# Optimization experiments

Measured on AMD Instinct MI355X. Metric: run time of the kernel, lower is better.

The kernel has to match this reference:

```python
import jax, jax.numpy as jnp
import numpy as np


def setup_inputs() -> dict:
    key = jax.random.key(0)
    ks = jax.random.split(key, 5)
    B, Cin, Cout, H, W, L, K = 16, 512, 512, 64, 64, 512, 3
    return {
        "content": jax.random.normal(ks[0], (B, Cin, H, W), jnp.float32),
        "latent": jax.random.normal(ks[1], (B, L), jnp.float32),
        "noise": jax.random.normal(ks[2], (B, 1, H, W), jnp.float32),
        "affine_w": jax.random.normal(ks[3], (Cin, L), jnp.float32),
        "affine_b": jnp.ones((Cin,), jnp.float32),  # ConvLayer fills affine bias with 1
        "conv_w": jax.random.normal(ks[4], (Cout, Cin, K, K), jnp.float32),
        "bias": jnp.zeros((1, Cout, 1, 1), jnp.float32),
        "noise_weight": jnp.asarray(0.1, jnp.float32),  # nonzero so noise path is exercised
    }


def reference(content, latent, noise, affine_w, affine_b, conv_w, bias, noise_weight):
    L = affine_w.shape[1]
    # affine (LinearLayer, lrelu=False): weight scaled by sqrt(1/inChannels), lrMultiplier=1
    style = latent @ (affine_w * np.sqrt(1.0 / L)).T + affine_b  # [B, Cin]
    # modulate: per-sample weights [B, Cout, Cin, k, k]
    w = conv_w[None] * style[:, None, :, None, None]
    # demodulate
    norm = jax.lax.rsqrt(jnp.sum(jnp.square(w), axis=(2, 3, 4), keepdims=True) + 1e-8)
    w = w * norm
    pad = conv_w.shape[-1] // 2
    # groups=batch trick == per-sample conv; vmap over batch
    def conv1(x, wk):  # x: [Cin,H,W], wk: [Cout,Cin,k,k]
        return jax.lax.conv_general_dilated(x[None], wk, (1, 1), [(pad, pad), (pad, pad)])[0]
    out = jax.vmap(conv1)(content, w)  # [B, Cout, H, W]
    out = out + noise_weight * noise
    out = jax.nn.leaky_relu(out + bias, negative_slope=0.2) * np.sqrt(2.0)
    return out
```

## Files before the change

### kernel.cpp

```cpp
#include <hip/hip_runtime.h>
#include <hip/hip_bf16.h>


typedef float f32x4 __attribute__((ext_vector_type(4)));
typedef float f32x16 __attribute__((ext_vector_type(16)));
typedef short bf16x8 __attribute__((ext_vector_type(8)));
typedef int i32x4 __attribute__((ext_vector_type(4)));

#define BB 16
#define CIN 512
#define COUT 512
#define HH 64
#define WW 64
#define LL 512

#define X3ROWB 2176
#define X3C16B (66 * X3ROWB)
#define X3BB (32 * X3C16B)
#define XS3_SZ (16 * X3BB)

#define WT3_STEPB 147456
#define WT3_SZ (32 * WT3_STEPB)

#define XS3_OFF 0
#define WT3_OFF XS3_SZ
#define STYLE_OFF (WT3_OFF + WT3_SZ)
#define STYLE_SZ (BB * CIN * 4)
#define WSQ_OFF (STYLE_OFF + STYLE_SZ)
#define WSQ_SZ (COUT * CIN * 4)
#define DEM_OFF (WSQ_OFF + WSQ_SZ)
#define DEM_SZ (BB * COUT * 4)
#define WS_NEEDED (DEM_OFF + DEM_SZ)

#define XSTEPB 22528
#define WSTEPB 18432

__device__ __forceinline__ void gld_lds16(const void* g, void* l) {
  __builtin_amdgcn_global_load_lds(
      (const __attribute__((address_space(1))) unsigned int*)g,
      (__attribute__((address_space(3))) unsigned int*)l, 16, 0, 0);
}

__global__ void style_kernel(const float* __restrict__ latent,
                             const float* __restrict__ affine_w,
                             const float* __restrict__ affine_b,
                             float* __restrict__ style) {
  const int idx = blockIdx.x * 256 + threadIdx.x;
  const int b = idx >> 9, ci = idx & 511;
  const float* lp = latent + b * LL;
  const float* wp = affine_w + ci * LL;
  float acc = 0.f;
  for (int l = 0; l < LL; ++l) acc += lp[l] * wp[l];
  style[idx] = acc * 0.044194173824159216f + affine_b[ci];
}

__global__ void wprep_kernel(const float* __restrict__ conv_w,
                             float* __restrict__ wsq,
                             __hip_bfloat16* __restrict__ wt3) {
  const int idx = blockIdx.x * 256 + threadIdx.x;
  const int co = idx >> 9, ci = idx & 511;
  const float* wp = conv_w + idx * 9;
  const int cib = ci >> 4, h = (ci >> 3) & 1, ci8 = ci & 7;
  __hip_bfloat16* base = wt3 + (size_t)cib * 73728 + h * 4096 + co * 8 + ci8;
  float ss = 0.f;
#pragma unroll
  for (int t = 0; t < 9; ++t) {
    float v = wp[t];
    ss += v * v;
    base[t * 8192] = __float2bfloat16(v);
  }
  wsq[idx] = ss;
}

__global__ void dem_kernel(const float* __restrict__ wsq,
                           const float* __restrict__ style,
                           float* __restrict__ dem) {
  const int idx = blockIdx.x * 256 + threadIdx.x;
  const int b = idx >> 9, co = idx & 511;
  const float* sp = style + b * CIN;
  const float* wp = wsq + co * CIN;
  float acc = 0.f;
  for (int ci = 0; ci < CIN; ++ci) {
    float s = sp[ci];
    acc += wp[ci] * s * s;
  }
  dem[idx] = 1.0f / sqrtf(acc + 1e-8f);
}

__global__ void xsprep_kernel(const float* __restrict__ content,
                              const float* __restrict__ style,
                              char* __restrict__ xs3) {
  __shared__ float tile[64][65];
  const int b = blockIdx.x >> 6;
  const int y = blockIdx.x & 63;
  const int tid = threadIdx.x;
  char* bbase = xs3 + (size_t)b * X3BB;

  {
    const int c16 = tid >> 3, rest = tid & 7;
    const int h = rest >> 2, pp = rest & 3;
    const int px = (pp == 0) ? 0 : 64 + pp;
    *(i32x4*)(bbase + (size_t)c16 * X3C16B + (y + 1) * X3ROWB + h * 1088 +
              px * 16) = (i32x4){0, 0, 0, 0};
  }
  if (y == 0 || y == 63) {
    const int rowidx = (y == 0) ? 0 : 65;
#pragma unroll
    for (int k = 0; k < 17; ++k) {
      const int u = tid + k * 256;
      if (u < 4352) {
        const int c16 = u / 136, w = u - c16 * 136;
        *(i32x4*)(bbase + (size_t)c16 * X3C16B + rowidx * X3ROWB + w * 16) =
            (i32x4){0, 0, 0, 0};
      }
    }
  }

  for (int cb = 0; cb < 8; ++cb) {
    const int ci0 = cb * 64;
    __syncthreads();
    {
      const int x = tid & 63;
      const int c0 = tid >> 6;
#pragma unroll
      for (int p = 0; p < 16; ++p) {
        const int ci = p * 4 + c0;
        tile[ci][x] = content[((b * CIN + ci0 + ci) * HH + y) * WW + x];
      }
    }
    __syncthreads();
    {
      const int x = tid & 63;
      const int o4 = tid >> 6;
#pragma unroll
      for (int oo = 0; oo < 2; ++oo) {
        const int oct = o4 * 2 + oo;
        const int c16 = cb * 4 + (oct >> 1);
        const int h = oct & 1;
        bf16x8 v;
#pragma unroll
        for (int j = 0; j < 8; ++j) {
          const float st = style[b * CIN + ci0 + oct * 8 + j];
          v[j] = __bfloat16_as_short(
              __float2bfloat16(tile[oct * 8 + j][x] * st));
        }
        *(bf16x8*)(bbase + (size_t)c16 * X3C16B + (y + 1) * X3ROWB + h * 1088 +
                   (x + 1) * 16) = v;
      }
    }
  }
}

__global__ __launch_bounds__(256, 2) void conv_kernel(
    const char* __restrict__ xs3,
    const char* __restrict__ wt3,
    const float* __restrict__ dem,
    const float* __restrict__ noise,
    const float* __restrict__ biasp,
    const float* __restrict__ nwp,
    float* __restrict__ out) {
  __shared__ __attribute__((aligned(16))) char xlds[2][XSTEPB];
  __shared__ __attribute__((aligned(16))) char wlds[2][WSTEPB];

  const int tid = threadIdx.x;
  const int lane = tid & 63;
  const int wv = tid >> 6;
  const int l31 = lane & 31;
  const int hsel = lane >> 5;

  const int d = blockIdx.x;
  const int L = (d & 7) * 128 + (d >> 3);
  const int cot = L & 7;
  const int yo = (L >> 3) & 7;
  const int b = L >> 6;
  const int co0 = cot << 6;
  const int y0 = yo << 3;

  const char* xsrc[6];
#pragma unroll
  for (int k = 0; k < 6; ++k) {
    const int c = wv + 4 * k;
    if (c < 22) {
      const int beta = c * 1024 + lane * 16;
      const int row = beta / X3ROWB;
      const int within = beta - row * X3ROWB;
      xsrc[k] = xs3 + (size_t)(b * 32) * X3C16B +
                (size_t)(y0 + row) * X3ROWB + within;
    } else {
      xsrc[k] = xs3;
    }
  }
  const char* wsrc[5];
#pragma unroll
  for (int k = 0; k < 5; ++k) {
    const int c = wv + 4 * k;
    if (c < 18) {
      const int tap = c >> 1, h = c & 1;
      wsrc[k] = wt3 + tap * 16384 + h * 8192 + (co0 + lane) * 16;
    } else {
      wsrc[k] = wt3;
    }
  }

  const int abase0 = hsel * 1024 + l31 * 16;
  const int bbase0 = hsel * 1088 + l31 * 16;
  const int xwrow = 2 * wv * X3ROWB;

  f32x16 acc[2][2][2];
#pragma unroll
  for (int mf = 0; mf < 2; ++mf)
#pragma unroll
    for (int r = 0; r < 2; ++r)
#pragma unroll
      for (int q = 0; q < 2; ++q)
#pragma unroll
        for (int e = 0; e < 16; ++e) acc[mf][r][q][e] = 0.f;

#define STG_X(K)                                                        \
  if ((K) < 5 || wv < 2)                                                \
    gld_lds16(xsrc[K] + xadv, xd + (wv + 4 * (K)) * 1024);
#define STG_W(K)                                                        \
  if ((K) < 4 || wv < 2)                                                \
    gld_lds16(wsrc[K] + wadv, wd + (wv + 4 * (K)) * 1024);

  {
    char* xd = xlds[0];
    char* wd = wlds[0];
    const size_t xadv = 0, wadv = 0;
    STG_X(0) STG_X(1) STG_X(2) STG_X(3) STG_X(4) STG_X(5)
    STG_W(0) STG_W(1) STG_W(2) STG_W(3) STG_W(4)
  }
  asm volatile("s_waitcnt vmcnt(0)" ::: "memory");
  __builtin_amdgcn_s_barrier();

#define PHASE(DX, STGPART, TAIL)                                          \
  {                                                                       \
    bf16x8 aP[3][2], bP[4][2];                                            \
    _Pragma("unroll") for (int dy = 0; dy < 3; ++dy)                      \
        _Pragma("unroll") for (int mf = 0; mf < 2; ++mf)                  \
            aP[dy][mf] = *(const bf16x8*)(wb + (dy * 3 + (DX)) * 2048 +   \
                                          abase0 + mf * 512);             \
    _Pragma("unroll") for (int ir = 0; ir < 4; ++ir)                      \
        _Pragma("unroll") for (int q = 0; q < 2; ++q)                     \
            bP[ir][q] = *(const bf16x8*)(xb + xwrow + ir * X3ROWB +       \
                                         bbase0 + (q * 32 + (DX)) * 16);  \
    if (t < 31) { STGPART }                                               \
    __builtin_amdgcn_s_barrier();                                         \
    asm volatile("s_waitcnt lgkmcnt(0)" ::: "memory");                    \
    __builtin_amdgcn_sched_barrier(0);                                    \
    __builtin_amdgcn_s_setprio(1);                                        \
    _Pragma("unroll") for (int ir = 0; ir < 4; ++ir)                      \
        _Pragma("unroll") for (int dy = 0; dy < 3; ++dy) {                \
      const int rr = ir - dy;                                             \
      if (rr == 0 || rr == 1) {                                           \
        _Pragma("unroll") for (int q = 0; q < 2; ++q)                     \
            _Pragma("unroll") for (int mf = 0; mf < 2; ++mf)              \
                acc[mf][rr][q] = __builtin_amdgcn_mfma_f32_32x32x16_bf16( \
                    aP[dy][mf], bP[ir][q], acc[mf][rr][q], 0, 0, 0);      \
      }                                                                   \
    }                                                                     \
    __builtin_amdgcn_s_setprio(0);                                        \
    TAIL;                                                                 \
    __builtin_amdgcn_s_barrier();                                         \
  }

  for (int t = 0; t < 32; ++t) {
    const int bi = t & 1;
    const char* xb = xlds[bi];
    const char* wb = wlds[bi];
    char* xd = xlds[bi ^ 1];
    char* wd = wlds[bi ^ 1];
    const size_t xadv = (size_t)(t + 1) * X3C16B;
    const size_t wadv = (size_t)(t + 1) * WT3_STEPB;

    PHASE(0, STG_X(0) STG_X(1) STG_W(0) STG_W(1), )
    PHASE(1, STG_X(2) STG_X(3) STG_W(2) STG_W(3), )
    PHASE(2, STG_X(4) STG_X(5) STG_W(4),
          asm volatile("s_waitcnt vmcnt(0)" ::: "memory"))
  }
#undef PHASE
#undef STG_X
#undef STG_W

  const float nwv = nwp[0];
  float nz[2][2];
#pragma unroll
  for (int r = 0; r < 2; ++r) {
    const int y = y0 + 2 * wv + r;
#pragma unroll
    for (int q = 0; q < 2; ++q)
      nz[r][q] = nwv * noise[(b << 12) + (y << 6) + q * 32 + l31];
  }
#pragma unroll
  for (int mf = 0; mf < 2; ++mf)
#pragma unroll
    for (int reg = 0; reg < 16; ++reg) {
      const int coo = (reg & 3) + 8 * (reg >> 2) + 4 * hsel;
      const int co = co0 + mf * 32 + coo;
      const float dv = dem[(b << 9) + co];
      const float bv = biasp[co];
#pragma unroll
      for (int r = 0; r < 2; ++r) {
        const int y = y0 + 2 * wv + r;
#pragma unroll
        for (int q = 0; q < 2; ++q) {
          float v = acc[mf][r][q][reg] * dv + nz[r][q] + bv;
          v = (v > 0.f ? v : 0.2f * v) * 1.41421356237309515f;
          out[(((size_t)(b << 9) + co) << 12) + (y << 6) + q * 32 + l31] = v;
        }
      }
    }
}

extern "C" void kernel_launch(void* const* d_in, const int* in_sizes, int n_in,
                              void* d_out, int out_size, void* d_ws, size_t ws_size,
                              hipStream_t stream) {
  const float* content  = (const float*)d_in[0];
  const float* latent   = (const float*)d_in[1];
  const float* noise    = (const float*)d_in[2];
  const float* affine_w = (const float*)d_in[3];
  const float* affine_b = (const float*)d_in[4];
  const float* conv_w   = (const float*)d_in[5];
  const float* bias     = (const float*)d_in[6];
  const float* nw       = (const float*)d_in[7];
  float* out = (float*)d_out;
  char* ws = (char*)d_ws;

  if (ws_size < (size_t)WS_NEEDED) return;

  char* xs3 = ws + XS3_OFF;
  __hip_bfloat16* wt3 = (__hip_bfloat16*)(ws + WT3_OFF);
  float* style = (float*)(ws + STYLE_OFF);
  float* wsq   = (float*)(ws + WSQ_OFF);
  float* dem   = (float*)(ws + DEM_OFF);

  style_kernel<<<dim3(32), dim3(256), 0, stream>>>(latent, affine_w, affine_b, style);
  wprep_kernel<<<dim3(1024), dim3(256), 0, stream>>>(conv_w, wsq, wt3);
  dem_kernel<<<dim3(32), dim3(256), 0, stream>>>(wsq, style, dem);
  xsprep_kernel<<<dim3(1024), dim3(256), 0, stream>>>(content, style, xs3);
  conv_kernel<<<dim3(1024), dim3(256), 0, stream>>>(
      xs3, (const char*)(ws + WT3_OFF), dem, noise, bias, nw, out);
}
```

Before: 316.6 us.

## Software-pipeline LDS fragment reads with register double buffering in conv loop

Restructures the main conv loop so LDS fragment reads for the next dx phase are issued into a second register set while MFMAs consume the current one. Partial lgkmcnt waits replace full drains. All global-to-LDS staging for a step is issued in one batch, and a barrier is dropped per phase. Launch bounds go from two blocks per CU to one, giving the compiler room for the extra fragment registers at the risk of lower occupancy and less latency hiding across blocks.

```diff
diff --git a/kernel.cpp b/kernel.cpp
--- a/kernel.cpp
+++ b/kernel.cpp
@@ -151,7 +151,7 @@
   }
 }
 
-__global__ __launch_bounds__(256, 2) void conv_kernel(
+__global__ __launch_bounds__(256, 1) void conv_kernel(
     const char* __restrict__ xs3,
     const char* __restrict__ wt3,
     const float* __restrict__ dem,
@@ -206,6 +206,11 @@
   const int bbase0 = hsel * 1088 + l31 * 16;
   const int xwrow = 2 * wv * X3ROWB;
 
+  const char* xb0 = xlds[0];
+  const char* wb0 = wlds[0];
+  const char* xb1 = xlds[1];
+  const char* wb1 = wlds[1];
+
   f32x16 acc[2][2][2];
 #pragma unroll
   for (int mf = 0; mf < 2; ++mf)
@@ -216,71 +221,113 @@
 #pragma unroll
         for (int e = 0; e < 16; ++e) acc[mf][r][q][e] = 0.f;
 
-#define STG_X(K)                                                        \
-  if ((K) < 5 || wv < 2)                                                \
-    gld_lds16(xsrc[K] + xadv, xd + (wv + 4 * (K)) * 1024);
-#define STG_W(K)                                                        \
-  if ((K) < 4 || wv < 2)                                                \
-    gld_lds16(wsrc[K] + wadv, wd + (wv + 4 * (K)) * 1024);
+#define STG_ALL                                                     \
+  {                                                                 \
+    _Pragma("unroll") for (int k = 0; k < 6; ++k) {                 \
+      const int c = wv + 4 * k;                                     \
+      if (c < 22) gld_lds16(xsrc[k] + xadv, xd + c * 1024);         \
+    }                                                               \
+    _Pragma("unroll") for (int k = 0; k < 5; ++k) {                 \
+      const int c = wv + 4 * k;                                     \
+      if (c < 18) gld_lds16(wsrc[k] + wadv, wd + c * 1024);         \
+    }                                                               \
+  }
+
+#define RDCL(AA, BB, XB, WB, DX)                                          \
+  {                                                                       \
+    _Pragma("unroll") for (int dy = 0; dy < 3; ++dy)                      \
+        _Pragma("unroll") for (int mf = 0; mf < 2; ++mf)                  \
+            AA[dy][mf] = *(const bf16x8*)((WB) + (dy * 3 + (DX)) * 2048 + \
+                                          abase0 + mf * 512);             \
+    _Pragma("unroll") for (int ir = 0; ir < 4; ++ir)                      \
+        _Pragma("unroll") for (int q = 0; q < 2; ++q)                     \
+            BB[ir][q] = *(const bf16x8*)((XB) + xwrow + ir * X3ROWB +     \
+                                         bbase0 + (q * 32 + (DX)) * 16);  \
+  }                                                                       \
+  __builtin_amdgcn_sched_barrier(0);
+
+#define MMCL(AA, BB)                                                      \
+  _Pragma("unroll") for (int ir = 0; ir < 4; ++ir)                        \
+      _Pragma("unroll") for (int dy = 0; dy < 3; ++dy) {                  \
+    const int rr = ir - dy;                                               \
+    if (rr == 0 || rr == 1) {                                             \
+      _Pragma("unroll") for (int q = 0; q < 2; ++q)                       \
+          _Pragma("unroll") for (int mf = 0; mf < 2; ++mf)                \
+              acc[mf][rr][q] = __builtin_amdgcn_mfma_f32_32x32x16_bf16(   \
+                  AA[dy][mf], BB[ir][q], acc[mf][rr][q], 0, 0, 0);        \
+    }                                                                     \
+  }
+
+#define W14                                                   \
+  asm volatile("s_waitcnt lgkmcnt(14)" ::: "memory");         \
+  __builtin_amdgcn_sched_barrier(0);
+#define WL0                                                   \
+  asm volatile("s_waitcnt lgkmcnt(0)" ::: "memory");          \
+  __builtin_amdgcn_sched_barrier(0);
+#define WV0 asm volatile("s_waitcnt vmcnt(0)" ::: "memory");
+#define BAR __builtin_amdgcn_s_barrier();
 
   {
     char* xd = xlds[0];
     char* wd = wlds[0];
     const size_t xadv = 0, wadv = 0;
-    STG_X(0) STG_X(1) STG_X(2) STG_X(3) STG_X(4) STG_X(5)
-    STG_W(0) STG_W(1) STG_W(2) STG_W(3) STG_W(4)
-  }
-  asm volatile("s_waitcnt vmcnt(0)" ::: "memory");
-  __builtin_amdgcn_s_barrier();
-
-#define PHASE(DX, STGPART, TAIL)                                          \
-  {                                                                       \
-    bf16x8 aP[3][2], bP[4][2];                                            \
-    _Pragma("unroll") for (int dy = 0; dy < 3; ++dy)                      \
-        _Pragma("unroll") for (int mf = 0; mf < 2; ++mf)                  \
-            aP[dy][mf] = *(const bf16x8*)(wb + (dy * 3 + (DX)) * 2048 +   \
-                                          abase0 + mf * 512);             \
-    _Pragma("unroll") for (int ir = 0; ir < 4; ++ir)                      \
-        _Pragma("unroll") for (int q = 0; q < 2; ++q)                     \
-            bP[ir][q] = *(const bf16x8*)(xb + xwrow + ir * X3ROWB +       \
-                                         bbase0 + (q * 32 + (DX)) * 16);  \
-    if (t < 31) { STGPART }                                               \
-    __builtin_amdgcn_s_barrier();                                         \
-    asm volatile("s_waitcnt lgkmcnt(0)" ::: "memory");                    \
-    __builtin_amdgcn_sched_barrier(0);                                    \
-    __builtin_amdgcn_s_setprio(1);                                        \
-    _Pragma("unroll") for (int ir = 0; ir < 4; ++ir)                      \
-        _Pragma("unroll") for (int dy = 0; dy < 3; ++dy) {                \
-      const int rr = ir - dy;                                             \
-      if (rr == 0 || rr == 1) {                                           \
-        _Pragma("unroll") for (int q = 0; q < 2; ++q)                     \
-            _Pragma("unroll") for (int mf = 0; mf < 2; ++mf)              \
-                acc[mf][rr][q] = __builtin_amdgcn_mfma_f32_32x32x16_bf16( \
-                    aP[dy][mf], bP[ir][q], acc[mf][rr][q], 0, 0, 0);      \
-      }                                                                   \
-    }                                                                     \
-    __builtin_amdgcn_s_setprio(0);                                        \
-    TAIL;                                                                 \
-    __builtin_amdgcn_s_barrier();                                         \
-  }
-
-  for (int t = 0; t < 32; ++t) {
-    const int bi = t & 1;
-    const char* xb = xlds[bi];
-    const char* wb = wlds[bi];
-    char* xd = xlds[bi ^ 1];
-    char* wd = wlds[bi ^ 1];
-    const size_t xadv = (size_t)(t + 1) * X3C16B;
-    const size_t wadv = (size_t)(t + 1) * WT3_STEPB;
-
-    PHASE(0, STG_X(0) STG_X(1) STG_W(0) STG_W(1), )
-    PHASE(1, STG_X(2) STG_X(3) STG_W(2) STG_W(3), )
-    PHASE(2, STG_X(4) STG_X(5) STG_W(4),
-          asm volatile("s_waitcnt vmcnt(0)" ::: "memory"))
-  }
-#undef PHASE
-#undef STG_X
-#undef STG_W
+    STG_ALL
+  }
+  WV0;
+  BAR;
+
+  bf16x8 a0[3][2], b0[4][2], a1[3][2], b1[4][2];
+  RDCL(a0, b0, xb0, wb0, 0)
+
+  for (int t = 0; t < 32; t += 2) {
+    RDCL(a1, b1, xb0, wb0, 1)
+    {
+      char* xd = xlds[1];
+      char* wd = wlds[1];
+      const size_t xadv = (size_t)(t + 1) * X3C16B;
+      const size_t wadv = (size_t)(t + 1) * WT3_STEPB;
+      STG_ALL
+    }
+    __builtin_amdgcn_sched_barrier(0);
+    W14 MMCL(a0, b0)
+    RDCL(a0, b0, xb0, wb0, 2)
+    W14 MMCL(a1, b1)
+    WV0;
+    BAR;
+    RDCL(a1, b1, xb1, wb1, 0)
+    W14 MMCL(a0, b0)
+    BAR;
+
+    RDCL(a0, b0, xb1, wb1, 1)
+    if (t < 30) {
+      char* xd = xlds[0];
+      char* wd = wlds[0];
+      const size_t xadv = (size_t)(t + 2) * X3C16B;
+      const size_t wadv = (size_t)(t + 2) * WT3_STEPB;
+      STG_ALL
+    }
+    __builtin_amdgcn_sched_barrier(0);
+    W14 MMCL(a1, b1)
+    RDCL(a1, b1, xb1, wb1, 2)
+    W14 MMCL(a0, b0)
+    WV0;
+    BAR;
+    if (t < 30) {
+      RDCL(a0, b0, xb0, wb0, 0)
+      W14
+    } else {
+      WL0
+    }
+    MMCL(a1, b1)
+    BAR;
+  }
+#undef STG_ALL
+#undef RDCL
+#undef MMCL
+#undef W14
+#undef WL0
+#undef WV0
+#undef BAR
 
   const float nwv = nwp[0];
   float nz[2][2];
```

Measured after the change: 327.7 us. 3.5% more time.

## Double conv block rows to 16 with 512 threads and rewrite xsprep without LDS

Applied to the files above, without the earlier changes.

The conv kernel now uses 512-thread blocks (8 waves) that each cover 16 output rows instead of 8, halving the grid. Each block stages 39 input-row chunks plus the weights, so the weight tile is shared across twice as many rows and the 2-row halo is amortised. All staging for the next step is issued in the first phase, not spread over three. The xsprep kernel drops its shared-memory transpose and reads content with strided loads directly. The cost is larger LDS per block, fewer blocks in flight, and uncoalesced-pattern changes in xsprep.

```diff
diff --git a/kernel.cpp b/kernel.cpp
--- a/kernel.cpp
+++ b/kernel.cpp
@@ -32,8 +32,11 @@
 #define DEM_SZ (BB * COUT * 4)
 #define WS_NEEDED (DEM_OFF + DEM_SZ)
 
-#define XSTEPB 22528
-#define WSTEPB 18432
+#define XCH 39
+#define XBUFB (XCH * 1024)
+#define WCH 18
+#define WBUFB (WCH * 1024)
+#define NCH (XCH + WCH)
 
 __device__ __forceinline__ void gld_lds16(const void* g, void* l) {
   __builtin_amdgcn_global_load_lds(
@@ -90,7 +93,6 @@
 __global__ void xsprep_kernel(const float* __restrict__ content,
                               const float* __restrict__ style,
                               char* __restrict__ xs3) {
-  __shared__ float tile[64][65];
   const int b = blockIdx.x >> 6;
   const int y = blockIdx.x & 63;
   const int tid = threadIdx.x;
@@ -99,9 +101,9 @@
   {
     const int c16 = tid >> 3, rest = tid & 7;
     const int h = rest >> 2, pp = rest & 3;
-    const int px = (pp == 0) ? 0 : 64 + pp;
+    const int pxp = (pp == 0) ? 0 : 64 + pp;
     *(i32x4*)(bbase + (size_t)c16 * X3C16B + (y + 1) * X3ROWB + h * 1088 +
-              px * 16) = (i32x4){0, 0, 0, 0};
+              pxp * 16) = (i32x4){0, 0, 0, 0};
   }
   if (y == 0 || y == 63) {
     const int rowidx = (y == 0) ? 0 : 65;
@@ -116,42 +118,22 @@
     }
   }
 
-  for (int cb = 0; cb < 8; ++cb) {
-    const int ci0 = cb * 64;
-    __syncthreads();
-    {
-      const int x = tid & 63;
-      const int c0 = tid >> 6;
-#pragma unroll
-      for (int p = 0; p < 16; ++p) {
-        const int ci = p * 4 + c0;
-        tile[ci][x] = content[((b * CIN + ci0 + ci) * HH + y) * WW + x];
-      }
-    }
-    __syncthreads();
-    {
-      const int x = tid & 63;
-      const int o4 = tid >> 6;
-#pragma unroll
-      for (int oo = 0; oo < 2; ++oo) {
-        const int oct = o4 * 2 + oo;
-        const int c16 = cb * 4 + (oct >> 1);
-        const int h = oct & 1;
-        bf16x8 v;
-#pragma unroll
-        for (int j = 0; j < 8; ++j) {
-          const float st = style[b * CIN + ci0 + oct * 8 + j];
-          v[j] = __bfloat16_as_short(
-              __float2bfloat16(tile[oct * 8 + j][x] * st));
-        }
-        *(bf16x8*)(bbase + (size_t)c16 * X3C16B + (y + 1) * X3ROWB + h * 1088 +
-                   (x + 1) * 16) = v;
-      }
-    }
-  }
-}
-
-__global__ __launch_bounds__(256, 2) void conv_kernel(
+  const int px = tid & 63;
+  const int wq = tid >> 6;
+  for (int oct = wq; oct < 64; oct += 4) {
+    const int c16 = oct >> 1, h = oct & 1;
+    const float* cp = content + ((size_t)(b * CIN + oct * 8) * HH + y) * WW + px;
+    const float* sp = style + b * CIN + oct * 8;
+    bf16x8 v;
+#pragma unroll
+    for (int j = 0; j < 8; ++j)
+      v[j] = __bfloat16_as_short(__float2bfloat16(cp[j * 4096] * sp[j]));
+    *(bf16x8*)(bbase + (size_t)c16 * X3C16B + (y + 1) * X3ROWB + h * 1088 +
+               (px + 1) * 16) = v;
+  }
+}
+
+__global__ __launch_bounds__(512, 2) void conv_kernel(
     const char* __restrict__ xs3,
     const char* __restrict__ wt3,
     const float* __restrict__ dem,
@@ -159,8 +141,8 @@
     const float* __restrict__ biasp,
     const float* __restrict__ nwp,
     float* __restrict__ out) {
-  __shared__ __attribute__((aligned(16))) char xlds[2][XSTEPB];
-  __shared__ __attribute__((aligned(16))) char wlds[2][WSTEPB];
+  __shared__ __attribute__((aligned(16))) char xlds[2][XBUFB];
+  __shared__ __attribute__((aligned(16))) char wlds[2][WBUFB];
 
   const int tid = threadIdx.x;
   const int lane = tid & 63;
@@ -169,37 +151,24 @@
   const int hsel = lane >> 5;
 
   const int d = blockIdx.x;
-  const int L = (d & 7) * 128 + (d >> 3);
+  const int L = (d & 7) * 64 + (d >> 3);
   const int cot = L & 7;
-  const int yo = (L >> 3) & 7;
-  const int b = L >> 6;
+  const int yo = (L >> 3) & 3;
+  const int b = L >> 5;
   const int co0 = cot << 6;
-  const int y0 = yo << 3;
-
-  const char* xsrc[6];
-#pragma unroll
-  for (int k = 0; k < 6; ++k) {
-    const int c = wv + 4 * k;
-    if (c < 22) {
-      const int beta = c * 1024 + lane * 16;
-      const int row = beta / X3ROWB;
-      const int within = beta - row * X3ROWB;
-      xsrc[k] = xs3 + (size_t)(b * 32) * X3C16B +
-                (size_t)(y0 + row) * X3ROWB + within;
-    } else {
-      xsrc[k] = xs3;
-    }
-  }
-  const char* wsrc[5];
-#pragma unroll
-  for (int k = 0; k < 5; ++k) {
-    const int c = wv + 4 * k;
-    if (c < 18) {
-      const int tap = c >> 1, h = c & 1;
-      wsrc[k] = wt3 + tap * 16384 + h * 8192 + (co0 + lane) * 16;
-    } else {
-      wsrc[k] = wt3;
-    }
+  const int y0 = yo << 4;
+
+  const char* gsrc[8];
+#pragma unroll
+  for (int k = 0; k < 8; ++k) {
+    const int c = wv + 8 * k;
+    if (c < XCH)
+      gsrc[k] = xs3 + (size_t)b * X3BB + (size_t)y0 * X3ROWB + c * 1024 +
+                lane * 16;
+    else if (c < NCH)
+      gsrc[k] = wt3 + (c - XCH) * 8192 + (co0 + lane) * 16;
+    else
+      gsrc[k] = xs3;
   }
 
   const int abase0 = hsel * 1024 + l31 * 16;
@@ -216,71 +185,63 @@
 #pragma unroll
         for (int e = 0; e < 16; ++e) acc[mf][r][q][e] = 0.f;
 
-#define STG_X(K)                                                        \
-  if ((K) < 5 || wv < 2)                                                \
-    gld_lds16(xsrc[K] + xadv, xd + (wv + 4 * (K)) * 1024);
-#define STG_W(K)                                                        \
-  if ((K) < 4 || wv < 2)                                                \
-    gld_lds16(wsrc[K] + wadv, wd + (wv + 4 * (K)) * 1024);
-
-  {
-    char* xd = xlds[0];
-    char* wd = wlds[0];
-    const size_t xadv = 0, wadv = 0;
-    STG_X(0) STG_X(1) STG_X(2) STG_X(3) STG_X(4) STG_X(5)
-    STG_W(0) STG_W(1) STG_W(2) STG_W(3) STG_W(4)
-  }
+#define STG_ALL(TT, BI)                                                    \
+  {                                                                        \
+    _Pragma("unroll") for (int k = 0; k < 8; ++k) {                        \
+      const int c = wv + 8 * k;                                            \
+      if (c < XCH)                                                         \
+        gld_lds16(gsrc[k] + (size_t)(TT) * X3C16B, xlds[BI] + c * 1024);   \
+      else if (c < NCH)                                                    \
+        gld_lds16(gsrc[k] + (size_t)(TT) * WT3_STEPB,                      \
+                  wlds[BI] + (c - XCH) * 1024);                            \
+    }                                                                      \
+  }
+
+#define PHASE(DX, DOSTG, DOVM)                                             \
+  {                                                                        \
+    bf16x8 aP[3][2], bP[4][2];                                             \
+    _Pragma("unroll") for (int dy = 0; dy < 3; ++dy)                       \
+        _Pragma("unroll") for (int mf = 0; mf < 2; ++mf)                   \
+            aP[dy][mf] = *(const bf16x8*)(wb + (dy * 3 + (DX)) * 2048 +    \
+                                          abase0 + mf * 512);              \
+    _Pragma("unroll") for (int ir = 0; ir < 4; ++ir)                       \
+        _Pragma("unroll") for (int q = 0; q < 2; ++q)                      \
+            bP[ir][q] = *(const bf16x8*)(xb + xwrow + ir * X3ROWB +        \
+                                         bbase0 + (q * 32 + (DX)) * 16);   \
+    if ((DOSTG) && t < 31) STG_ALL(t + 1, bi ^ 1)                          \
+    __builtin_amdgcn_s_barrier();                                          \
+    asm volatile("s_waitcnt lgkmcnt(0)" ::: "memory");                     \
+    __builtin_amdgcn_sched_barrier(0);                                     \
+    __builtin_amdgcn_s_setprio(1);                                         \
+    _Pragma("unroll") for (int ir = 0; ir < 4; ++ir)                       \
+        _Pragma("unroll") for (int dy = 0; dy < 3; ++dy) {                 \
+      const int rr = ir - dy;                                              \
+      if (rr == 0 || rr == 1) {                                            \
+        _Pragma("unroll") for (int q = 0; q < 2; ++q)                      \
+            _Pragma("unroll") for (int mf = 0; mf < 2; ++mf)               \
+                acc[mf][rr][q] = __builtin_amdgcn_mfma_f32_32x32x16_bf16(  \
+                    aP[dy][mf], bP[ir][q], acc[mf][rr][q], 0, 0, 0);       \
+      }                                                                    \
+    }                                                                      \
+    __builtin_amdgcn_s_setprio(0);                                         \
+    if (DOVM) asm volatile("s_waitcnt vmcnt(0)" ::: "memory");             \
+    __builtin_amdgcn_s_barrier();                                          \
+  }
+
+  STG_ALL(0, 0)
   asm volatile("s_waitcnt vmcnt(0)" ::: "memory");
   __builtin_amdgcn_s_barrier();
-
-#define PHASE(DX, STGPART, TAIL)                                          \
-  {                                                                       \
-    bf16x8 aP[3][2], bP[4][2];                                            \
-    _Pragma("unroll") for (int dy = 0; dy < 3; ++dy)                      \
-        _Pragma("unroll") for (int mf = 0; mf < 2; ++mf)                  \
-            aP[dy][mf] = *(const bf16x8*)(wb + (dy * 3 + (DX)) * 2048 +   \
-                                          abase0 + mf * 512);             \
-    _Pragma("unroll") for (int ir = 0; ir < 4; ++ir)                      \
-        _Pragma("unroll") for (int q = 0; q < 2; ++q)                     \
-            bP[ir][q] = *(const bf16x8*)(xb + xwrow + ir * X3ROWB +       \
-                                         bbase0 + (q * 32 + (DX)) * 16);  \
-    if (t < 31) { STGPART }                                               \
-    __builtin_amdgcn_s_barrier();                                         \
-    asm volatile("s_waitcnt lgkmcnt(0)" ::: "memory");                    \
-    __builtin_amdgcn_sched_barrier(0);                                    \
-    __builtin_amdgcn_s_setprio(1);                                        \
-    _Pragma("unroll") for (int ir = 0; ir < 4; ++ir)                      \
-        _Pragma("unroll") for (int dy = 0; dy < 3; ++dy) {                \
-      const int rr = ir - dy;                                             \
-      if (rr == 0 || rr == 1) {                                           \
-        _Pragma("unroll") for (int q = 0; q < 2; ++q)                     \
-            _Pragma("unroll") for (int mf = 0; mf < 2; ++mf)              \
-                acc[mf][rr][q] = __builtin_amdgcn_mfma_f32_32x32x16_bf16( \
-                    aP[dy][mf], bP[ir][q], acc[mf][rr][q], 0, 0, 0);      \
-      }                                                                   \
-    }                                                                     \
-    __builtin_amdgcn_s_setprio(0);                                        \
-    TAIL;                                                                 \
-    __builtin_amdgcn_s_barrier();                                         \
-  }
 
   for (int t = 0; t < 32; ++t) {
     const int bi = t & 1;
     const char* xb = xlds[bi];
     const char* wb = wlds[bi];
-    char* xd = xlds[bi ^ 1];
-    char* wd = wlds[bi ^ 1];
-    const size_t xadv = (size_t)(t + 1) * X3C16B;
-    const size_t wadv = (size_t)(t + 1) * WT3_STEPB;
-
-    PHASE(0, STG_X(0) STG_X(1) STG_W(0) STG_W(1), )
-    PHASE(1, STG_X(2) STG_X(3) STG_W(2) STG_W(3), )
-    PHASE(2, STG_X(4) STG_X(5) STG_W(4),
-          asm volatile("s_waitcnt vmcnt(0)" ::: "memory"))
+    PHASE(0, 1, 0)
+    PHASE(1, 0, 0)
+    PHASE(2, 0, 1)
   }
 #undef PHASE
-#undef STG_X
-#undef STG_W
+#undef STG_ALL
 
   const float nwv = nwp[0];
   float nz[2][2];
@@ -338,6 +299,6 @@
   wprep_kernel<<<dim3(1024), dim3(256), 0, stream>>>(conv_w, wsq, wt3);
   dem_kernel<<<dim3(32), dim3(256), 0, stream>>>(wsq, style, dem);
   xsprep_kernel<<<dim3(1024), dim3(256), 0, stream>>>(content, style, xs3);
-  conv_kernel<<<dim3(1024), dim3(256), 0, stream>>>(
+  conv_kernel<<<dim3(512), dim3(512), 0, stream>>>(
       xs3, (const char*)(ws + WT3_OFF), dem, noise, bias, nw, out);
 }
```

After: 331.2 us. 1.05x slower.
